# Kernel tuning notes

Hardware: AMD Instinct MI355X
Metric: run time of the kernel (lower is better)

Reference implementation:

```python
import jax, jax.numpy as jnp
import numpy as np
from jax import lax

# Dense emulation of the irregular graph stage (repo helpers img2graph /
# IrregularMaxPool2d / GraphConv2d): nodes = pixels of the stride-4 grid.
# Where pooling_mask==1, a 2x2 block is max-pooled (pooled value replicated
# over the block) and subsequent GraphConv2d gathers neighbors with offset 2
# (dilation 2); where mask==0 the node keeps resolution and offset 1.


def _conv(x, w, b, dil=1):
    p = dil  # SAME padding for a 3x3 kernel with dilation `dil`
    y = lax.conv_general_dilated(x, w, (1, 1), ((p, p), (p, p)),
                                 rhs_dilation=(dil, dil),
                                 dimension_numbers=('NCHW', 'OIHW', 'NCHW'))
    return y + b[None, :, None, None]


def _maxpool2(x):
    return lax.reduce_window(x, -jnp.inf, lax.max, (1, 1, 2, 2), (1, 1, 2, 2), 'VALID')


def _up2(x):
    return jnp.repeat(jnp.repeat(x, 2, axis=2), 2, axis=3)


def setup_inputs() -> dict:
    key = jax.random.key(0)
    ks = jax.random.split(key, 12)
    B, H, W = 4, 384, 384
    inp = {
        'batch': jax.random.normal(ks[0], (B, 3, H, W), jnp.float32),
        'pooling_mask': jax.random.randint(ks[1], (B, 1, H // 8, W // 8), 0, 2, jnp.int32),
    }
    cfg = [(3, 64), (64, 64), (64, 128), (128, 128), (128, 256),
           (256, 256), (256, 256), (256, 512), (512, 512), (512, 512)]
    for i, (cin, cout) in enumerate(cfg):
        scale = float(np.sqrt(2.0 / (cin * 9)))  # He init for 3x3 conv
        inp[f'W{i+1}'] = jax.random.normal(ks[2 + (i % 10)], (cout, cin, 3, 3), jnp.float32) * scale
        inp[f'b{i+1}'] = jnp.zeros((cout,), jnp.float32)
    return inp


def reference(batch, pooling_mask, W1, b1, W2, b2, W3, b3, W4, b4, W5, b5,
              W6, b6, W7, b7, W8, b8, W9, b9, W10, b10):
    x = jax.nn.relu(_conv(batch, W1, b1))
    x = jax.nn.relu(_conv(x, W2, b2))
    x = _maxpool2(x)                                  # H/2
    x = jax.nn.relu(_conv(x, W3, b3))
    x = jax.nn.relu(_conv(x, W4, b4))
    x = _maxpool2(x)                                  # H/4 (OS4)
    x = jax.nn.relu(_conv(x, W5, b5))
    x = jax.nn.relu(_conv(x, W6, b6))
    x = jax.nn.relu(_conv(x, W7, b7))
    # img2graph + IrregularMaxPool2d (number_pools=1)
    m = (pooling_mask > 0).astype(x.dtype)            # [B,1,H/8,W/8]
    m_up = _up2(m)                                    # [B,1,H/4,W/4]
    x = m_up * _up2(_maxpool2(x)) + (1.0 - m_up) * x  # pool 2x2 where mask==1

    # GraphConv2d: per-node neighbor offset = 1 + mask (spatially varying dilation)
    def gconv(h, w, b):
        return m_up * _conv(h, w, b, dil=2) + (1.0 - m_up) * _conv(h, w, b, dil=1)

    x = jax.nn.relu(gconv(x, W8, b8))
    x = jax.nn.relu(gconv(x, W9, b9))
    x = jax.nn.relu(gconv(x, W10, b10))               # use_relu=True
    return x  # graph2img: nodes already laid out on the stride-4 grid
```

## Files before the change

kernel.cpp:

```cpp
#include <hip/hip_runtime.h>


typedef __attribute__((ext_vector_type(8))) short short8;
typedef __attribute__((ext_vector_type(4))) float f32x4;

__device__ __forceinline__ float b2f(ushort u) {
    return __uint_as_float(((unsigned)u) << 16);
}
__device__ __forceinline__ ushort f2b(float f) {
    unsigned x = __float_as_uint(f);
    x += 0x7FFFu + ((x >> 16) & 1u);
    return (ushort)(x >> 16);
}
__device__ __forceinline__ ushort bmax(ushort a, ushort b) {
    return b2f(a) > b2f(b) ? a : b;
}

__global__ __launch_bounds__(256)
void repack_w(const float* __restrict__ w, ushort* __restrict__ wp, int Cin, int Cout)
{
    int n = Cout * Cin * 9;
    int i = blockIdx.x * 256 + threadIdx.x;
    if (i >= n) return;
    int CBl = Cin / 32;
    int c8   = i & 7;
    int co   = (i >> 3) % Cout;
    int rest = (i >> 3) / Cout;
    int q    = rest & 3;
    int cbt  = rest >> 2;
    int cb   = cbt % CBl;
    int t    = cbt / CBl;
    int ci   = cb * 32 + q * 8 + c8;
    wp[i] = f2b(w[((size_t)co * Cin + ci) * 9 + t]);
}

__global__ __launch_bounds__(256)
void l1_conv(const float* __restrict__ in, const float* __restrict__ w,
             const float* __restrict__ bias, ushort* __restrict__ out)
{
    const int H = 384, W = 384;
    __shared__ float s[3][18][18];
    const int tid = threadIdx.x;
    const int tilesX = W / 16;
    const int x0 = (blockIdx.x % tilesX) * 16;
    const int y0 = (blockIdx.x / tilesX) * 16;
    const int b  = blockIdx.z;

    for (int i = tid; i < 3 * 18 * 18; i += 256) {
        int ci = i / (18 * 18);
        int r  = i % (18 * 18);
        int iy = r / 18, ix = r % 18;
        int gy = y0 - 1 + iy, gx = x0 - 1 + ix;
        float v = 0.f;
        if ((unsigned)gy < (unsigned)H && (unsigned)gx < (unsigned)W)
            v = in[((size_t)(b * 3 + ci) * H + gy) * W + gx];
        s[ci][iy][ix] = v;
    }
    __syncthreads();

    const int tx = tid & 15, ty = tid >> 4;
    float iv[3][3][3];
    #pragma unroll
    for (int ci = 0; ci < 3; ++ci)
        #pragma unroll
        for (int ky = 0; ky < 3; ++ky)
            #pragma unroll
            for (int kx = 0; kx < 3; ++kx)
                iv[ci][ky][kx] = s[ci][ty + ky][tx + kx];

    size_t pix = ((size_t)(b * H + y0 + ty) * W + x0 + tx);
    #pragma unroll
    for (int c4 = 0; c4 < 4; ++c4) {
        __align__(16) ushort ob[16];
        #pragma unroll
        for (int co = 0; co < 16; ++co) {
            int coG = c4 * 16 + co;
            float a = bias[coG];
            #pragma unroll
            for (int ci = 0; ci < 3; ++ci)
                #pragma unroll
                for (int ky = 0; ky < 3; ++ky)
                    #pragma unroll
                    for (int kx = 0; kx < 3; ++kx)
                        a = fmaf(w[((size_t)coG * 3 + ci) * 9 + ky * 3 + kx],
                                 iv[ci][ky][kx], a);
            a = a > 0.f ? a : 0.f;
            ob[co] = f2b(a);
        }
        *(short8*)&out[pix * 64 + c4 * 16]     = *(short8*)&ob[0];
        *(short8*)&out[pix * 64 + c4 * 16 + 8] = *(short8*)&ob[8];
    }
}

__global__ __launch_bounds__(256)
void maxpool_nhwc(const ushort* __restrict__ in, ushort* __restrict__ out,
                  int Ho, int Wo, int C)
{
    int n = 4 * Ho * Wo * (C / 8);
    int i = blockIdx.x * 256 + threadIdx.x;
    if (i >= n) return;
    int c8 = i % (C / 8);
    int pi = i / (C / 8);
    int x = pi % Wo, y = (pi / Wo) % Ho, b = pi / (Wo * Ho);
    int Hi = Ho * 2, Wi = Wo * 2;
    const ushort* p = in + ((size_t)(b * Hi + 2 * y) * Wi + 2 * x) * C + c8 * 8;
    short8 v00 = *(const short8*)p;
    short8 v01 = *(const short8*)(p + C);
    short8 v10 = *(const short8*)(p + (size_t)Wi * C);
    short8 v11 = *(const short8*)(p + (size_t)Wi * C + C);
    short8 o;
    #pragma unroll
    for (int j = 0; j < 8; ++j)
        o[j] = (short)bmax(bmax((ushort)v00[j], (ushort)v01[j]),
                           bmax((ushort)v10[j], (ushort)v11[j]));
    *(short8*)(out + (size_t)i * 8) = o;
}

__global__ __launch_bounds__(256)
void irpool_nhwc(const ushort* __restrict__ in, const int* __restrict__ mask,
                 ushort* __restrict__ out)
{
    const int C = 256, H = 96, Wd = 96;
    int n = 4 * H * Wd * (C / 8);
    int i = blockIdx.x * 256 + threadIdx.x;
    if (i >= n) return;
    int c8 = i % (C / 8);
    int pi = i / (C / 8);
    int x = pi % Wd, y = (pi / Wd) % H, b = pi / (Wd * H);
    int m = mask[(b * 48 + (y >> 1)) * 48 + (x >> 1)];
    short8 o;
    if (m) {
        int y0 = y & ~1, x0 = x & ~1;
        const ushort* p = in + ((size_t)(b * H + y0) * Wd + x0) * C + c8 * 8;
        short8 v00 = *(const short8*)p;
        short8 v01 = *(const short8*)(p + C);
        short8 v10 = *(const short8*)(p + (size_t)Wd * C);
        short8 v11 = *(const short8*)(p + (size_t)Wd * C + C);
        #pragma unroll
        for (int j = 0; j < 8; ++j)
            o[j] = (short)bmax(bmax((ushort)v00[j], (ushort)v01[j]),
                               bmax((ushort)v10[j], (ushort)v11[j]));
    } else {
        o = *(const short8*)(in + (size_t)pi * C + c8 * 8);
    }
    *(short8*)(out + (size_t)pi * C + c8 * 8) = o;
}

template<int TR, int BN, int CIN, int COUT, int H, int W, bool GCONV, bool FINAL>
__global__ __launch_bounds__(256)
void conv_mfma(const ushort* __restrict__ in, const ushort* __restrict__ wp,
               const float* __restrict__ bias, void* __restrict__ outv,
               const int* __restrict__ mask)
{
    constexpr int BM   = TR * 16;
    constexpr int CB   = CIN / 32;
    constexpr int HA   = GCONV ? 2 : 1;
    constexpr int CW   = 16 + 2 * HA;
    constexpr int CR   = TR + 2 * HA;
    constexpr int NCH  = CR * CW;
    constexpr int NCHP = NCH + 2;
    constexpr int WM   = BM / 64;
    constexpr int NSA  = NCH * 4;
    constexpr int NSLA = (NSA + 255) / 256;
    constexpr int NSB  = 12 * BN;
    constexpr int NSLB = NSB / 256;
    static_assert(NSB % 256 == 0, "B staging must tile 256 threads");

    __shared__ __align__(16) ushort sA[4 * NCHP * 8];
    __shared__ __align__(16) ushort sB[12 * BN * 8];

    const int tid  = threadIdx.x;
    const int lane = tid & 63;
    const int wv   = tid >> 6;
    const int wm   = wv % WM;
    const int wn   = wv / WM;
    const int col  = lane & 15;
    const int quad = lane >> 4;

    const int tiles_x = W / 16, tiles_y = H / TR;
    int sp = blockIdx.x;
    const int b  = sp / (tiles_x * tiles_y);
    int rr = sp - b * tiles_x * tiles_y;
    const int ty = rr / tiles_x;
    const int tx = rr - ty * tiles_x;
    const int y0 = ty * TR, x0 = tx * 16;
    const int co0 = blockIdx.y * BN;

    int dA[4], aoff[4];
    #pragma unroll
    for (int mt = 0; mt < 4; ++mt) {
        dA[mt] = 1;
        if (GCONV) {
            int y = y0 + wm * 4 + mt, x = x0 + col;
            dA[mt] = mask[(b * (H / 2) + (y >> 1)) * (W / 2) + (x >> 1)] ? 2 : 1;
        }
        aoff[mt] = (HA + wm * 4 + mt) * CW + HA + col;
    }

    short8 pA[NSLA];
    short8 pB[NSLB];

    auto loadA = [&](int cb) {
        #pragma unroll
        for (int k = 0; k < NSLA; ++k) {
            int i = tid + k * 256;
            short8 v = {0, 0, 0, 0, 0, 0, 0, 0};
            if (NSA == NSLA * 256 || i < NSA) {
                int chunk = i >> 2, part = i & 3;
                int yy = chunk / CW, xx = chunk - yy * CW;
                int gy = y0 - HA + yy, gx = x0 - HA + xx;
                if ((unsigned)gy < (unsigned)H && (unsigned)gx < (unsigned)W)
                    v = *(const short8*)(in + ((size_t)(b * H + gy) * W + gx) * CIN
                                         + cb * 32 + part * 8);
            }
            pA[k] = v;
        }
    };
    auto storeA = [&]() {
        #pragma unroll
        for (int k = 0; k < NSLA; ++k) {
            int i = tid + k * 256;
            if (NSA == NSLA * 256 || i < NSA) {
                int chunk = i >> 2, part = i & 3;
                *(short8*)&sA[(part * NCHP + chunk) * 8] = pA[k];
            }
        }
    };
    auto loadB = [&](int s) {
        int cb = s / 3, row = s % 3;
        #pragma unroll
        for (int k = 0; k < NSLB; ++k) {
            int i = tid + k * 256;
            int co = i % BN;
            int rq = i / BN;
            const ushort* gp = wp
                + (((size_t)(row * 3 + (rq >> 2)) * CB + cb) * 4 + (rq & 3))
                      * COUT * 8
                + (size_t)(co0 + co) * 8;
            pB[k] = *(const short8*)gp;
        }
    };
    auto storeB = [&]() {
        #pragma unroll
        for (int k = 0; k < NSLB; ++k) {
            int i = tid + k * 256;
            *(short8*)&sB[(size_t)i * 8] = pB[k];
        }
    };

    f32x4 acc[4][4];
    #pragma unroll
    for (int i = 0; i < 4; ++i)
        #pragma unroll
        for (int j = 0; j < 4; ++j)
            acc[i][j] = (f32x4){0.f, 0.f, 0.f, 0.f};

    loadA(0);
    loadB(0);
    storeA();
    storeB();
    __syncthreads();

    for (int s = 0; s < 3 * CB; ++s) {
        const int row  = s % 3;
        const bool last = (s == 3 * CB - 1);
        if (!last) {
            loadB(s + 1);
            if (row == 2) loadA(s / 3 + 1);
        }
        const int ky = row - 1;
        #pragma unroll
        for (int j = 0; j < 3; ++j) {
            const int kx = j - 1;
            short8 af[4], bf4[4];
            #pragma unroll
            for (int i = 0; i < 4; ++i) {
                int chunk = aoff[i] + dA[i] * (ky * CW + kx);
                af[i]  = *(const short8*)&sA[(quad * NCHP + chunk) * 8];
                bf4[i] = *(const short8*)&sB[((j * 4 + quad) * BN
                                              + wn * 64 + i * 16 + col) * 8];
            }
            #pragma unroll
            for (int mt = 0; mt < 4; ++mt)
                #pragma unroll
                for (int nt = 0; nt < 4; ++nt)
                    acc[mt][nt] = __builtin_amdgcn_mfma_f32_16x16x32_bf16(
                        af[mt], bf4[nt], acc[mt][nt], 0, 0, 0);
        }
        if (!last) {
            __syncthreads();
            storeB();
            if (row == 2) storeA();
            __syncthreads();
        }
    }

    if (!FINAL) {
        ushort* outp = (ushort*)outv;
        #pragma unroll
        for (int mt = 0; mt < 4; ++mt) {
            int y = y0 + wm * 4 + mt;
            #pragma unroll
            for (int nt = 0; nt < 4; ++nt) {
                int co = co0 + wn * 64 + nt * 16 + col;
                float bv = bias[co];
                #pragma unroll
                for (int r2 = 0; r2 < 4; ++r2) {
                    int x = x0 + quad * 4 + r2;
                    float vv = acc[mt][nt][r2] + bv;
                    vv = vv > 0.f ? vv : 0.f;
                    outp[((size_t)(b * H + y) * W + x) * COUT + co] = f2b(vv);
                }
            }
        }
    } else {
        float* outp = (float*)outv;
        #pragma unroll
        for (int mt = 0; mt < 4; ++mt) {
            int y = y0 + wm * 4 + mt;
            #pragma unroll
            for (int nt = 0; nt < 4; ++nt) {
                int co = co0 + wn * 64 + nt * 16 + col;
                float bv = bias[co];
                f32x4 vv;
                #pragma unroll
                for (int r2 = 0; r2 < 4; ++r2) {
                    float z = acc[mt][nt][r2] + bv;
                    vv[r2] = z > 0.f ? z : 0.f;
                }
                *(f32x4*)&outp[((size_t)(b * COUT + co) * H + y) * W + x0 + quad * 4] = vv;
            }
        }
    }
}

extern "C" void kernel_launch(void* const* d_in, const int* in_sizes, int n_in,
                              void* d_out, int out_size, void* d_ws, size_t ws_size,
                              hipStream_t stream)
{
    const float* x    = (const float*)d_in[0];
    const int*   mask = (const int*)d_in[1];
    const float* Wt[10];
    const float* bs[10];
    for (int i = 0; i < 10; ++i) {
        Wt[i] = (const float*)d_in[2 + 2 * i];
        bs[i] = (const float*)d_in[3 + 2 * i];
    }

    const size_t ACT = (size_t)4 * 384 * 384 * 64;
    ushort* A  = (ushort*)d_ws;
    ushort* Bb = A + ACT;
    ushort* wpbase = Bb + ACT;

    static const int cins[10]  = {3, 64, 64, 128, 128, 256, 256, 256, 512, 512};
    static const int couts[10] = {64, 64, 128, 128, 256, 256, 256, 512, 512, 512};
    ushort* wp[10];
    size_t wo = 0;
    for (int l = 1; l < 10; ++l) {
        wp[l] = wpbase + wo;
        wo += (size_t)couts[l] * cins[l] * 9;
    }
    for (int l = 1; l < 10; ++l) {
        int n = couts[l] * cins[l] * 9;
        repack_w<<<(n + 255) / 256, 256, 0, stream>>>(Wt[l], wp[l], cins[l], couts[l]);
    }

    l1_conv<<<dim3(24 * 24, 1, 4), 256, 0, stream>>>(x, Wt[0], bs[0], A);

    conv_mfma<16, 64, 64, 64, 384, 384, false, false>
        <<<dim3(4 * 24 * 24, 1), 256, 0, stream>>>(A, wp[1], bs[1], Bb, nullptr);
    maxpool_nhwc<<<(4 * 192 * 192 * 8 + 255) / 256, 256, 0, stream>>>(Bb, A, 192, 192, 64);

    conv_mfma<8, 128, 64, 128, 192, 192, false, false>
        <<<dim3(4 * 24 * 12, 1), 256, 0, stream>>>(A, wp[2], bs[2], Bb, nullptr);
    conv_mfma<8, 128, 128, 128, 192, 192, false, false>
        <<<dim3(4 * 24 * 12, 1), 256, 0, stream>>>(Bb, wp[3], bs[3], A, nullptr);
    maxpool_nhwc<<<(4 * 96 * 96 * 16 + 255) / 256, 256, 0, stream>>>(A, Bb, 96, 96, 128);

    conv_mfma<8, 128, 128, 256, 96, 96, false, false>
        <<<dim3(4 * 12 * 6, 2), 256, 0, stream>>>(Bb, wp[4], bs[4], A, nullptr);
    conv_mfma<8, 128, 256, 256, 96, 96, false, false>
        <<<dim3(4 * 12 * 6, 2), 256, 0, stream>>>(A, wp[5], bs[5], Bb, nullptr);
    conv_mfma<8, 128, 256, 256, 96, 96, false, false>
        <<<dim3(4 * 12 * 6, 2), 256, 0, stream>>>(Bb, wp[6], bs[6], A, nullptr);

    irpool_nhwc<<<(4 * 96 * 96 * 32 + 255) / 256, 256, 0, stream>>>(A, mask, Bb);

    conv_mfma<8, 128, 256, 512, 96, 96, true, false>
        <<<dim3(4 * 12 * 6, 4), 256, 0, stream>>>(Bb, wp[7], bs[7], A, mask);
    conv_mfma<8, 128, 512, 512, 96, 96, true, false>
        <<<dim3(4 * 12 * 6, 4), 256, 0, stream>>>(A, wp[8], bs[8], Bb, mask);
    conv_mfma<8, 128, 512, 512, 96, 96, true, true>
        <<<dim3(4 * 12 * 6, 4), 256, 0, stream>>>(Bb, wp[9], bs[9], d_out, mask);

    (void)in_sizes; (void)n_in; (void)out_size; (void)ws_size;
}
```

Measured before the change: 957.3 us.

## Load conv weights directly from global into registers, drop shared-memory B staging

Removes the shared-memory staging buffer for weights. Each wave now loads its MFMA B fragments straight from global memory into registers, double-buffered one tap ahead. The loop is restructured to process pairs of input-channel blocks with all 9 taps unrolled, so block-wide barriers only occur at A-tile refills rather than after every kernel row. This cuts LDS traffic and synchronisation, but weights are now fetched redundantly by waves that share output channels (relying on L1/L2), and global-load latency is exposed with only one tap of lookahead.

```diff
diff --git a/kernel.cpp b/kernel.cpp
--- a/kernel.cpp
+++ b/kernel.cpp
@@ -154,6 +154,7 @@
 {
     constexpr int BM   = TR * 16;
     constexpr int CB   = CIN / 32;
+    static_assert(CB % 2 == 0, "cb-pair unroll needs even CB");
     constexpr int HA   = GCONV ? 2 : 1;
     constexpr int CW   = 16 + 2 * HA;
     constexpr int CR   = TR + 2 * HA;
@@ -162,12 +163,8 @@
     constexpr int WM   = BM / 64;
     constexpr int NSA  = NCH * 4;
     constexpr int NSLA = (NSA + 255) / 256;
-    constexpr int NSB  = 12 * BN;
-    constexpr int NSLB = NSB / 256;
-    static_assert(NSB % 256 == 0, "B staging must tile 256 threads");
 
     __shared__ __align__(16) ushort sA[4 * NCHP * 8];
-    __shared__ __align__(16) ushort sB[12 * BN * 8];
 
     const int tid  = threadIdx.x;
     const int lane = tid & 63;
@@ -197,8 +194,9 @@
         aoff[mt] = (HA + wm * 4 + mt) * CW + HA + col;
     }
 
+    const ushort* wbase = wp + ((size_t)quad * COUT + co0 + wn * 64 + col) * 8;
+
     short8 pA[NSLA];
-    short8 pB[NSLB];
 
     auto loadA = [&](int cb) {
         #pragma unroll
@@ -226,26 +224,13 @@
             }
         }
     };
-    auto loadB = [&](int s) {
-        int cb = s / 3, row = s % 3;
-        #pragma unroll
-        for (int k = 0; k < NSLB; ++k) {
-            int i = tid + k * 256;
-            int co = i % BN;
-            int rq = i / BN;
-            const ushort* gp = wp
-                + (((size_t)(row * 3 + (rq >> 2)) * CB + cb) * 4 + (rq & 3))
-                      * COUT * 8
-                + (size_t)(co0 + co) * 8;
-            pB[k] = *(const short8*)gp;
-        }
-    };
-    auto storeB = [&]() {
-        #pragma unroll
-        for (int k = 0; k < NSLB; ++k) {
-            int i = tid + k * 256;
-            *(short8*)&sB[(size_t)i * 8] = pB[k];
-        }
+
+    short8 bfa[4], bfb[4];
+    auto loadBF = [&](int t, int cb, short8 (&dst)[4]) {
+        size_t ofs = (size_t)(t * CB + cb) * 4 * COUT * 8;
+        #pragma unroll
+        for (int nt = 0; nt < 4; ++nt)
+            dst[nt] = *(const short8*)(wbase + ofs + nt * 128);
     };
 
     f32x4 acc[4][4];
@@ -256,41 +241,48 @@
             acc[i][j] = (f32x4){0.f, 0.f, 0.f, 0.f};
 
     loadA(0);
-    loadB(0);
     storeA();
-    storeB();
+    loadBF(0, 0, bfa);
     __syncthreads();
 
-    for (int s = 0; s < 3 * CB; ++s) {
-        const int row  = s % 3;
-        const bool last = (s == 3 * CB - 1);
-        if (!last) {
-            loadB(s + 1);
-            if (row == 2) loadA(s / 3 + 1);
-        }
-        const int ky = row - 1;
-        #pragma unroll
-        for (int j = 0; j < 3; ++j) {
-            const int kx = j - 1;
-            short8 af[4], bf4[4];
+    for (int cb2 = 0; cb2 < CB; cb2 += 2) {
+        loadA(cb2 + 1);
+        #pragma unroll
+        for (int g = 0; g < 18; ++g) {
+            const int tt = (g >= 9) ? g - 9 : g;
+            if (g == 9) {
+                __syncthreads();
+                storeA();
+                __syncthreads();
+                if (cb2 + 2 < CB) loadA(cb2 + 2);
+            }
+            {
+                int gn = g + 1;
+                int cbn = cb2 + (gn >= 9 ? 1 : 0);
+                int tn  = (gn >= 9) ? gn - 9 : gn;
+                if (gn == 18) { cbn = cb2 + 2; tn = 0; }
+                if (cbn < CB) {
+                    if ((g & 1) == 0) loadBF(tn, cbn, bfb);
+                    else              loadBF(tn, cbn, bfa);
+                }
+            }
+            const int ky = tt / 3 - 1, kx = tt % 3 - 1;
+            short8 af[4];
             #pragma unroll
             for (int i = 0; i < 4; ++i) {
                 int chunk = aoff[i] + dA[i] * (ky * CW + kx);
-                af[i]  = *(const short8*)&sA[(quad * NCHP + chunk) * 8];
-                bf4[i] = *(const short8*)&sB[((j * 4 + quad) * BN
-                                              + wn * 64 + i * 16 + col) * 8];
+                af[i] = *(const short8*)&sA[(quad * NCHP + chunk) * 8];
             }
             #pragma unroll
             for (int mt = 0; mt < 4; ++mt)
                 #pragma unroll
                 for (int nt = 0; nt < 4; ++nt)
                     acc[mt][nt] = __builtin_amdgcn_mfma_f32_16x16x32_bf16(
-                        af[mt], bf4[nt], acc[mt][nt], 0, 0, 0);
-        }
-        if (!last) {
+                        af[mt], (g & 1) ? bfb[nt] : bfa[nt], acc[mt][nt], 0, 0, 0);
+        }
+        if (cb2 + 2 < CB) {
             __syncthreads();
-            storeB();
-            if (row == 2) storeA();
+            storeA();
             __syncthreads();
         }
     }
```

Result: slower. 1.114 ms (+16.4%).

## Schedule conv tiles dynamically via per-layer atomic work counters

Applied to the files above, without the earlier changes.

Turns the MFMA conv kernel into a loop in which each block claims output tiles from a global atomic counter instead of deriving its tile from blockIdx. Per-layer counters live in the workspace and are zeroed by a new tiny kernel. The launch grids equal the tile counts, so in practice each block claims about one tile plus a final failing claim. The intent is smoother load balance and dispatch order; the cost is an extra atomic and barrier per tile and a kernel-wide loop that may raise register pressure.

```diff
diff --git a/kernel.cpp b/kernel.cpp
--- a/kernel.cpp
+++ b/kernel.cpp
@@ -15,6 +15,8 @@
 __device__ __forceinline__ ushort bmax(ushort a, ushort b) {
     return b2f(a) > b2f(b) ? a : b;
 }
+
+__global__ void zero_counters(int* __restrict__ c) { c[threadIdx.x] = 0; }
 
 __global__ __launch_bounds__(256)
 void repack_w(const float* __restrict__ w, ushort* __restrict__ wp, int Cin, int Cout)
@@ -150,7 +152,7 @@
 __global__ __launch_bounds__(256)
 void conv_mfma(const ushort* __restrict__ in, const ushort* __restrict__ wp,
                const float* __restrict__ bias, void* __restrict__ outv,
-               const int* __restrict__ mask)
+               const int* __restrict__ mask, int* __restrict__ counter)
 {
     constexpr int BM   = TR * 16;
     constexpr int CB   = CIN / 32;
@@ -165,9 +167,13 @@
     constexpr int NSB  = 12 * BN;
     constexpr int NSLB = NSB / 256;
     static_assert(NSB % 256 == 0, "B staging must tile 256 threads");
+    constexpr int NSP    = 4 * (H / TR) * (W / 16);
+    constexpr int NSLAB  = COUT / BN;
+    constexpr int NTILES = NSP * NSLAB;
 
     __shared__ __align__(16) ushort sA[4 * NCHP * 8];
     __shared__ __align__(16) ushort sB[12 * BN * 8];
+    __shared__ int s_tile;
 
     const int tid  = threadIdx.x;
     const int lane = tid & 63;
@@ -176,159 +182,166 @@
     const int wn   = wv / WM;
     const int col  = lane & 15;
     const int quad = lane >> 4;
-
     const int tiles_x = W / 16, tiles_y = H / TR;
-    int sp = blockIdx.x;
-    const int b  = sp / (tiles_x * tiles_y);
-    int rr = sp - b * tiles_x * tiles_y;
-    const int ty = rr / tiles_x;
-    const int tx = rr - ty * tiles_x;
-    const int y0 = ty * TR, x0 = tx * 16;
-    const int co0 = blockIdx.y * BN;
-
-    int dA[4], aoff[4];
-    #pragma unroll
-    for (int mt = 0; mt < 4; ++mt) {
-        dA[mt] = 1;
-        if (GCONV) {
-            int y = y0 + wm * 4 + mt, x = x0 + col;
-            dA[mt] = mask[(b * (H / 2) + (y >> 1)) * (W / 2) + (x >> 1)] ? 2 : 1;
-        }
-        aoff[mt] = (HA + wm * 4 + mt) * CW + HA + col;
-    }
-
-    short8 pA[NSLA];
-    short8 pB[NSLB];
-
-    auto loadA = [&](int cb) {
-        #pragma unroll
-        for (int k = 0; k < NSLA; ++k) {
-            int i = tid + k * 256;
-            short8 v = {0, 0, 0, 0, 0, 0, 0, 0};
-            if (NSA == NSLA * 256 || i < NSA) {
-                int chunk = i >> 2, part = i & 3;
-                int yy = chunk / CW, xx = chunk - yy * CW;
-                int gy = y0 - HA + yy, gx = x0 - HA + xx;
-                if ((unsigned)gy < (unsigned)H && (unsigned)gx < (unsigned)W)
-                    v = *(const short8*)(in + ((size_t)(b * H + gy) * W + gx) * CIN
-                                         + cb * 32 + part * 8);
-            }
-            pA[k] = v;
-        }
-    };
-    auto storeA = [&]() {
-        #pragma unroll
-        for (int k = 0; k < NSLA; ++k) {
-            int i = tid + k * 256;
-            if (NSA == NSLA * 256 || i < NSA) {
-                int chunk = i >> 2, part = i & 3;
-                *(short8*)&sA[(part * NCHP + chunk) * 8] = pA[k];
-            }
-        }
-    };
-    auto loadB = [&](int s) {
-        int cb = s / 3, row = s % 3;
-        #pragma unroll
-        for (int k = 0; k < NSLB; ++k) {
-            int i = tid + k * 256;
-            int co = i % BN;
-            int rq = i / BN;
-            const ushort* gp = wp
-                + (((size_t)(row * 3 + (rq >> 2)) * CB + cb) * 4 + (rq & 3))
-                      * COUT * 8
-                + (size_t)(co0 + co) * 8;
-            pB[k] = *(const short8*)gp;
-        }
-    };
-    auto storeB = [&]() {
-        #pragma unroll
-        for (int k = 0; k < NSLB; ++k) {
-            int i = tid + k * 256;
-            *(short8*)&sB[(size_t)i * 8] = pB[k];
-        }
-    };
-
-    f32x4 acc[4][4];
-    #pragma unroll
-    for (int i = 0; i < 4; ++i)
-        #pragma unroll
-        for (int j = 0; j < 4; ++j)
-            acc[i][j] = (f32x4){0.f, 0.f, 0.f, 0.f};
-
-    loadA(0);
-    loadB(0);
-    storeA();
-    storeB();
-    __syncthreads();
-
-    for (int s = 0; s < 3 * CB; ++s) {
-        const int row  = s % 3;
-        const bool last = (s == 3 * CB - 1);
-        if (!last) {
-            loadB(s + 1);
-            if (row == 2) loadA(s / 3 + 1);
-        }
-        const int ky = row - 1;
-        #pragma unroll
-        for (int j = 0; j < 3; ++j) {
-            const int kx = j - 1;
-            short8 af[4], bf4[4];
-            #pragma unroll
-            for (int i = 0; i < 4; ++i) {
-                int chunk = aoff[i] + dA[i] * (ky * CW + kx);
-                af[i]  = *(const short8*)&sA[(quad * NCHP + chunk) * 8];
-                bf4[i] = *(const short8*)&sB[((j * 4 + quad) * BN
-                                              + wn * 64 + i * 16 + col) * 8];
-            }
-            #pragma unroll
-            for (int mt = 0; mt < 4; ++mt)
-                #pragma unroll
-                for (int nt = 0; nt < 4; ++nt)
-                    acc[mt][nt] = __builtin_amdgcn_mfma_f32_16x16x32_bf16(
-                        af[mt], bf4[nt], acc[mt][nt], 0, 0, 0);
-        }
-        if (!last) {
-            __syncthreads();
-            storeB();
-            if (row == 2) storeA();
-            __syncthreads();
-        }
-    }
-
-    if (!FINAL) {
-        ushort* outp = (ushort*)outv;
+
+    while (true) {
+        if (tid == 0) s_tile = atomicAdd(counter, 1);
+        __syncthreads();
+        const int t = s_tile;
+        if (t >= NTILES) break;
+
+        const int sp  = t % NSP;
+        const int co0 = (t / NSP) * BN;
+        const int b  = sp / (tiles_x * tiles_y);
+        int rr = sp - b * tiles_x * tiles_y;
+        const int ty = rr / tiles_x;
+        const int tx = rr - ty * tiles_x;
+        const int y0 = ty * TR, x0 = tx * 16;
+
+        int dA[4], aoff[4];
         #pragma unroll
         for (int mt = 0; mt < 4; ++mt) {
-            int y = y0 + wm * 4 + mt;
-            #pragma unroll
-            for (int nt = 0; nt < 4; ++nt) {
-                int co = co0 + wn * 64 + nt * 16 + col;
-                float bv = bias[co];
+            dA[mt] = 1;
+            if (GCONV) {
+                int y = y0 + wm * 4 + mt, x = x0 + col;
+                dA[mt] = mask[(b * (H / 2) + (y >> 1)) * (W / 2) + (x >> 1)] ? 2 : 1;
+            }
+            aoff[mt] = (HA + wm * 4 + mt) * CW + HA + col;
+        }
+
+        short8 pA[NSLA];
+        short8 pB[NSLB];
+
+        auto loadA = [&](int cb) {
+            #pragma unroll
+            for (int k = 0; k < NSLA; ++k) {
+                int i = tid + k * 256;
+                short8 v = {0, 0, 0, 0, 0, 0, 0, 0};
+                if (NSA == NSLA * 256 || i < NSA) {
+                    int chunk = i >> 2, part = i & 3;
+                    int yy = chunk / CW, xx = chunk - yy * CW;
+                    int gy = y0 - HA + yy, gx = x0 - HA + xx;
+                    if ((unsigned)gy < (unsigned)H && (unsigned)gx < (unsigned)W)
+                        v = *(const short8*)(in + ((size_t)(b * H + gy) * W + gx) * CIN
+                                             + cb * 32 + part * 8);
+                }
+                pA[k] = v;
+            }
+        };
+        auto storeA = [&]() {
+            #pragma unroll
+            for (int k = 0; k < NSLA; ++k) {
+                int i = tid + k * 256;
+                if (NSA == NSLA * 256 || i < NSA) {
+                    int chunk = i >> 2, part = i & 3;
+                    *(short8*)&sA[(part * NCHP + chunk) * 8] = pA[k];
+                }
+            }
+        };
+        auto loadB = [&](int s) {
+            int cb = s / 3, row = s % 3;
+            #pragma unroll
+            for (int k = 0; k < NSLB; ++k) {
+                int i = tid + k * 256;
+                int co = i % BN;
+                int rq = i / BN;
+                const ushort* gp = wp
+                    + (((size_t)(row * 3 + (rq >> 2)) * CB + cb) * 4 + (rq & 3))
+                          * COUT * 8
+                    + (size_t)(co0 + co) * 8;
+                pB[k] = *(const short8*)gp;
+            }
+        };
+        auto storeB = [&]() {
+            #pragma unroll
+            for (int k = 0; k < NSLB; ++k) {
+                int i = tid + k * 256;
+                *(short8*)&sB[(size_t)i * 8] = pB[k];
+            }
+        };
+
+        f32x4 acc[4][4];
+        #pragma unroll
+        for (int i = 0; i < 4; ++i)
+            #pragma unroll
+            for (int j = 0; j < 4; ++j)
+                acc[i][j] = (f32x4){0.f, 0.f, 0.f, 0.f};
+
+        loadA(0);
+        loadB(0);
+        storeA();
+        storeB();
+        __syncthreads();
+
+        for (int s = 0; s < 3 * CB; ++s) {
+            const int row  = s % 3;
+            const bool last = (s == 3 * CB - 1);
+            if (!last) {
+                loadB(s + 1);
+                if (row == 2) loadA(s / 3 + 1);
+            }
+            const int ky = row - 1;
+            #pragma unroll
+            for (int j = 0; j < 3; ++j) {
+                const int kx = j - 1;
+                short8 af[4], bf4[4];
                 #pragma unroll
-                for (int r2 = 0; r2 < 4; ++r2) {
-                    int x = x0 + quad * 4 + r2;
-                    float vv = acc[mt][nt][r2] + bv;
-                    vv = vv > 0.f ? vv : 0.f;
-                    outp[((size_t)(b * H + y) * W + x) * COUT + co] = f2b(vv);
+                for (int i = 0; i < 4; ++i) {
+                    int chunk = aoff[i] + dA[i] * (ky * CW + kx);
+                    af[i]  = *(const short8*)&sA[(quad * NCHP + chunk) * 8];
+                    bf4[i] = *(const short8*)&sB[((j * 4 + quad) * BN
+                                                  + wn * 64 + i * 16 + col) * 8];
                 }
+                #pragma unroll
+                for (int mt = 0; mt < 4; ++mt)
+                    #pragma unroll
+                    for (int nt = 0; nt < 4; ++nt)
+                        acc[mt][nt] = __builtin_amdgcn_mfma_f32_16x16x32_bf16(
+                            af[mt], bf4[nt], acc[mt][nt], 0, 0, 0);
+            }
+            if (!last) {
+                __syncthreads();
+                storeB();
+                if (row == 2) storeA();
+                __syncthreads();
             }
         }
-    } else {
-        float* outp = (float*)outv;
-        #pragma unroll
-        for (int mt = 0; mt < 4; ++mt) {
-            int y = y0 + wm * 4 + mt;
-            #pragma unroll
-            for (int nt = 0; nt < 4; ++nt) {
-                int co = co0 + wn * 64 + nt * 16 + col;
-                float bv = bias[co];
-                f32x4 vv;
+
+        if (!FINAL) {
+            ushort* outp = (ushort*)outv;
+            #pragma unroll
+            for (int mt = 0; mt < 4; ++mt) {
+                int y = y0 + wm * 4 + mt;
                 #pragma unroll
-                for (int r2 = 0; r2 < 4; ++r2) {
-                    float z = acc[mt][nt][r2] + bv;
-                    vv[r2] = z > 0.f ? z : 0.f;
+                for (int nt = 0; nt < 4; ++nt) {
+                    int co = co0 + wn * 64 + nt * 16 + col;
+                    float bv = bias[co];
+                    #pragma unroll
+                    for (int r2 = 0; r2 < 4; ++r2) {
+                        int x = x0 + quad * 4 + r2;
+                        float vv = acc[mt][nt][r2] + bv;
+                        vv = vv > 0.f ? vv : 0.f;
+                        outp[((size_t)(b * H + y) * W + x) * COUT + co] = f2b(vv);
+                    }
                 }
-                *(f32x4*)&outp[((size_t)(b * COUT + co) * H + y) * W + x0 + quad * 4] = vv;
+            }
+        } else {
+            float* outp = (float*)outv;
+            #pragma unroll
+            for (int mt = 0; mt < 4; ++mt) {
+                int y = y0 + wm * 4 + mt;
+                #pragma unroll
+                for (int nt = 0; nt < 4; ++nt) {
+                    int co = co0 + wn * 64 + nt * 16 + col;
+                    float bv = bias[co];
+                    f32x4 vv;
+                    #pragma unroll
+                    for (int r2 = 0; r2 < 4; ++r2) {
+                        float z = acc[mt][nt][r2] + bv;
+                        vv[r2] = z > 0.f ? z : 0.f;
+                    }
+                    *(f32x4*)&outp[((size_t)(b * COUT + co) * H + y) * W + x0 + quad * 4] = vv;
+                }
             }
         }
     }
@@ -360,38 +373,41 @@
         wp[l] = wpbase + wo;
         wo += (size_t)couts[l] * cins[l] * 9;
     }
+    int* counters = (int*)(wpbase + ((wo + 1) & ~(size_t)1));
+
     for (int l = 1; l < 10; ++l) {
         int n = couts[l] * cins[l] * 9;
         repack_w<<<(n + 255) / 256, 256, 0, stream>>>(Wt[l], wp[l], cins[l], couts[l]);
     }
+    zero_counters<<<1, 16, 0, stream>>>(counters);
 
     l1_conv<<<dim3(24 * 24, 1, 4), 256, 0, stream>>>(x, Wt[0], bs[0], A);
 
     conv_mfma<16, 64, 64, 64, 384, 384, false, false>
-        <<<dim3(4 * 24 * 24, 1), 256, 0, stream>>>(A, wp[1], bs[1], Bb, nullptr);
+        <<<dim3(2304), 256, 0, stream>>>(A, wp[1], bs[1], Bb, nullptr, counters + 0);
     maxpool_nhwc<<<(4 * 192 * 192 * 8 + 255) / 256, 256, 0, stream>>>(Bb, A, 192, 192, 64);
 
     conv_mfma<8, 128, 64, 128, 192, 192, false, false>
-        <<<dim3(4 * 24 * 12, 1), 256, 0, stream>>>(A, wp[2], bs[2], Bb, nullptr);
+        <<<dim3(1152), 256, 0, stream>>>(A, wp[2], bs[2], Bb, nullptr, counters + 1);
     conv_mfma<8, 128, 128, 128, 192, 192, false, false>
-        <<<dim3(4 * 24 * 12, 1), 256, 0, stream>>>(Bb, wp[3], bs[3], A, nullptr);
+        <<<dim3(1152), 256, 0, stream>>>(Bb, wp[3], bs[3], A, nullptr, counters + 2);
     maxpool_nhwc<<<(4 * 96 * 96 * 16 + 255) / 256, 256, 0, stream>>>(A, Bb, 96, 96, 128);
 
     conv_mfma<8, 128, 128, 256, 96, 96, false, false>
-        <<<dim3(4 * 12 * 6, 2), 256, 0, stream>>>(Bb, wp[4], bs[4], A, nullptr);
+        <<<dim3(576), 256, 0, stream>>>(Bb, wp[4], bs[4], A, nullptr, counters + 3);
     conv_mfma<8, 128, 256, 256, 96, 96, false, false>
-        <<<dim3(4 * 12 * 6, 2), 256, 0, stream>>>(A, wp[5], bs[5], Bb, nullptr);
+        <<<dim3(576), 256, 0, stream>>>(A, wp[5], bs[5], Bb, nullptr, counters + 4);
     conv_mfma<8, 128, 256, 256, 96, 96, false, false>
-        <<<dim3(4 * 12 * 6, 2), 256, 0, stream>>>(Bb, wp[6], bs[6], A, nullptr);
+        <<<dim3(576), 256, 0, stream>>>(Bb, wp[6], bs[6], A, nullptr, counters + 5);
 
     irpool_nhwc<<<(4 * 96 * 96 * 32 + 255) / 256, 256, 0, stream>>>(A, mask, Bb);
 
     conv_mfma<8, 128, 256, 512, 96, 96, true, false>
-        <<<dim3(4 * 12 * 6, 4), 256, 0, stream>>>(Bb, wp[7], bs[7], A, mask);
+        <<<dim3(1152), 256, 0, stream>>>(Bb, wp[7], bs[7], A, mask, counters + 6);
     conv_mfma<8, 128, 512, 512, 96, 96, true, false>
-        <<<dim3(4 * 12 * 6, 4), 256, 0, stream>>>(A, wp[8], bs[8], Bb, mask);
+        <<<dim3(1152), 256, 0, stream>>>(A, wp[8], bs[8], Bb, mask, counters + 7);
     conv_mfma<8, 128, 512, 512, 96, 96, true, true>
-        <<<dim3(4 * 12 * 6, 4), 256, 0, stream>>>(Bb, wp[9], bs[9], d_out, mask);
+        <<<dim3(1152), 256, 0, stream>>>(Bb, wp[9], bs[9], d_out, mask, counters + 8);
 
     (void)in_sizes; (void)n_in; (void)out_size; (void)ws_size;
 }
```

New measurement: 1.017 ms. 1.06x slower.

## Fuse maxpool and irregular pool into conv epilogues; batch weight repacks

Applied to the files above, without the earlier changes.

Removes the separate maxpool and irregular-pool kernels by doing the 2x2 max inside the conv epilogue. Each wave's accumulator tile already covers aligned 2x2 pixel blocks, and the mask is read per block for the irregular pool. It also merges the nine per-layer weight repack launches into one kernel that takes a struct of per-layer pointers and offsets. This saves full activation round-trips through memory and several kernel launches, at the cost of scattered 2-byte stores in the pooled epilogue.

```diff
diff --git a/kernel.cpp b/kernel.cpp
--- a/kernel.cpp
+++ b/kernel.cpp
@@ -15,23 +15,36 @@
 __device__ __forceinline__ ushort bmax(ushort a, ushort b) {
     return b2f(a) > b2f(b) ? a : b;
 }
+__device__ __forceinline__ float fmaxf2(float a, float b) { return a > b ? a : b; }
+
+struct RepackArgs {
+    const float* w[9];
+    ushort*      wp[9];
+    int cin[9];
+    int cout[9];
+    int off[10];
+};
 
 __global__ __launch_bounds__(256)
-void repack_w(const float* __restrict__ w, ushort* __restrict__ wp, int Cin, int Cout)
+void repack_all(RepackArgs a)
 {
-    int n = Cout * Cin * 9;
     int i = blockIdx.x * 256 + threadIdx.x;
-    if (i >= n) return;
-    int CBl = Cin / 32;
-    int c8   = i & 7;
-    int co   = (i >> 3) % Cout;
-    int rest = (i >> 3) / Cout;
+    if (i >= a.off[9]) return;
+    int l = 0;
+    #pragma unroll
+    for (int k = 1; k < 9; ++k) l += (i >= a.off[k]);
+    int j = i - a.off[l];
+    int Cin = a.cin[l], Cout = a.cout[l];
+    int CBl  = Cin / 32;
+    int c8   = j & 7;
+    int co   = (j >> 3) % Cout;
+    int rest = (j >> 3) / Cout;
     int q    = rest & 3;
     int cbt  = rest >> 2;
     int cb   = cbt % CBl;
     int t    = cbt / CBl;
     int ci   = cb * 32 + q * 8 + c8;
-    wp[i] = f2b(w[((size_t)co * Cin + ci) * 9 + t]);
+    a.wp[l][j] = f2b(a.w[l][((size_t)co * Cin + ci) * 9 + t]);
 }
 
 __global__ __launch_bounds__(256)
@@ -92,61 +105,8 @@
     }
 }
 
-__global__ __launch_bounds__(256)
-void maxpool_nhwc(const ushort* __restrict__ in, ushort* __restrict__ out,
-                  int Ho, int Wo, int C)
-{
-    int n = 4 * Ho * Wo * (C / 8);
-    int i = blockIdx.x * 256 + threadIdx.x;
-    if (i >= n) return;
-    int c8 = i % (C / 8);
-    int pi = i / (C / 8);
-    int x = pi % Wo, y = (pi / Wo) % Ho, b = pi / (Wo * Ho);
-    int Hi = Ho * 2, Wi = Wo * 2;
-    const ushort* p = in + ((size_t)(b * Hi + 2 * y) * Wi + 2 * x) * C + c8 * 8;
-    short8 v00 = *(const short8*)p;
-    short8 v01 = *(const short8*)(p + C);
-    short8 v10 = *(const short8*)(p + (size_t)Wi * C);
-    short8 v11 = *(const short8*)(p + (size_t)Wi * C + C);
-    short8 o;
-    #pragma unroll
-    for (int j = 0; j < 8; ++j)
-        o[j] = (short)bmax(bmax((ushort)v00[j], (ushort)v01[j]),
-                           bmax((ushort)v10[j], (ushort)v11[j]));
-    *(short8*)(out + (size_t)i * 8) = o;
-}
-
-__global__ __launch_bounds__(256)
-void irpool_nhwc(const ushort* __restrict__ in, const int* __restrict__ mask,
-                 ushort* __restrict__ out)
-{
-    const int C = 256, H = 96, Wd = 96;
-    int n = 4 * H * Wd * (C / 8);
-    int i = blockIdx.x * 256 + threadIdx.x;
-    if (i >= n) return;
-    int c8 = i % (C / 8);
-    int pi = i / (C / 8);
-    int x = pi % Wd, y = (pi / Wd) % H, b = pi / (Wd * H);
-    int m = mask[(b * 48 + (y >> 1)) * 48 + (x >> 1)];
-    short8 o;
-    if (m) {
-        int y0 = y & ~1, x0 = x & ~1;
-        const ushort* p = in + ((size_t)(b * H + y0) * Wd + x0) * C + c8 * 8;
-        short8 v00 = *(const short8*)p;
-        short8 v01 = *(const short8*)(p + C);
-        short8 v10 = *(const short8*)(p + (size_t)Wd * C);
-        short8 v11 = *(const short8*)(p + (size_t)Wd * C + C);
-        #pragma unroll
-        for (int j = 0; j < 8; ++j)
-            o[j] = (short)bmax(bmax((ushort)v00[j], (ushort)v01[j]),
-                               bmax((ushort)v10[j], (ushort)v11[j]));
-    } else {
-        o = *(const short8*)(in + (size_t)pi * C + c8 * 8);
-    }
-    *(short8*)(out + (size_t)pi * C + c8 * 8) = o;
-}
-
-template<int TR, int BN, int CIN, int COUT, int H, int W, bool GCONV, bool FINAL>
+template<int TR, int BN, int CIN, int COUT, int H, int W, bool GCONV, bool FINAL,
+         int POOL>
 __global__ __launch_bounds__(256)
 void conv_mfma(const ushort* __restrict__ in, const ushort* __restrict__ wp,
                const float* __restrict__ bias, void* __restrict__ outv,
@@ -295,7 +255,25 @@
         }
     }
 
-    if (!FINAL) {
+    if (FINAL) {
+        float* outp = (float*)outv;
+        #pragma unroll
+        for (int mt = 0; mt < 4; ++mt) {
+            int y = y0 + wm * 4 + mt;
+            #pragma unroll
+            for (int nt = 0; nt < 4; ++nt) {
+                int co = co0 + wn * 64 + nt * 16 + col;
+                float bv = bias[co];
+                f32x4 vv;
+                #pragma unroll
+                for (int r2 = 0; r2 < 4; ++r2) {
+                    float z = acc[mt][nt][r2] + bv;
+                    vv[r2] = z > 0.f ? z : 0.f;
+                }
+                *(f32x4*)&outp[((size_t)(b * COUT + co) * H + y) * W + x0 + quad * 4] = vv;
+            }
+        }
+    } else if (POOL == 0) {
         ushort* outp = (ushort*)outv;
         #pragma unroll
         for (int mt = 0; mt < 4; ++mt) {
@@ -313,22 +291,66 @@
                 }
             }
         }
-    } else {
-        float* outp = (float*)outv;
-        #pragma unroll
-        for (int mt = 0; mt < 4; ++mt) {
-            int y = y0 + wm * 4 + mt;
-            #pragma unroll
-            for (int nt = 0; nt < 4; ++nt) {
-                int co = co0 + wn * 64 + nt * 16 + col;
-                float bv = bias[co];
-                f32x4 vv;
+    } else if (POOL == 1) {
+        ushort* outp = (ushort*)outv;
+        #pragma unroll
+        for (int nt = 0; nt < 4; ++nt) {
+            int co = co0 + wn * 64 + nt * 16 + col;
+            float bv = bias[co];
+            float v[4][4];
+            #pragma unroll
+            for (int mt = 0; mt < 4; ++mt)
                 #pragma unroll
                 for (int r2 = 0; r2 < 4; ++r2) {
                     float z = acc[mt][nt][r2] + bv;
-                    vv[r2] = z > 0.f ? z : 0.f;
-                }
-                *(f32x4*)&outp[((size_t)(b * COUT + co) * H + y) * W + x0 + quad * 4] = vv;
+                    v[mt][r2] = z > 0.f ? z : 0.f;
+                }
+            #pragma unroll
+            for (int mt2 = 0; mt2 < 2; ++mt2) {
+                int yp = (y0 >> 1) + wm * 2 + mt2;
+                #pragma unroll
+                for (int j = 0; j < 2; ++j) {
+                    int xp = (x0 >> 1) + quad * 2 + j;
+                    float m = fmaxf2(fmaxf2(v[2*mt2][2*j],   v[2*mt2][2*j+1]),
+                                     fmaxf2(v[2*mt2+1][2*j], v[2*mt2+1][2*j+1]));
+                    outp[((size_t)(b * (H/2) + yp) * (W/2) + xp) * COUT + co] = f2b(m);
+                }
+            }
+        }
+    } else {
+        ushort* outp = (ushort*)outv;
+        int mc[2][2];
+        #pragma unroll
+        for (int my = 0; my < 2; ++my)
+            #pragma unroll
+            for (int mx = 0; mx < 2; ++mx) {
+                int y = y0 + wm * 4 + my * 2;
+                int x = x0 + quad * 4 + mx * 2;
+                mc[my][mx] = mask[(b * (H / 2) + (y >> 1)) * (W / 2) + (x >> 1)];
+            }
+        #pragma unroll
+        for (int nt = 0; nt < 4; ++nt) {
+            int co = co0 + wn * 64 + nt * 16 + col;
+            float bv = bias[co];
+            float v[4][4];
+            #pragma unroll
+            for (int mt = 0; mt < 4; ++mt)
+                #pragma unroll
+                for (int r2 = 0; r2 < 4; ++r2) {
+                    float z = acc[mt][nt][r2] + bv;
+                    v[mt][r2] = z > 0.f ? z : 0.f;
+                }
+            #pragma unroll
+            for (int mt = 0; mt < 4; ++mt) {
+                int y = y0 + wm * 4 + mt;
+                #pragma unroll
+                for (int r2 = 0; r2 < 4; ++r2) {
+                    int x = x0 + quad * 4 + r2;
+                    float p = fmaxf2(fmaxf2(v[mt][r2],     v[mt][r2 ^ 1]),
+                                     fmaxf2(v[mt ^ 1][r2], v[mt ^ 1][r2 ^ 1]));
+                    float o = mc[mt >> 1][r2 >> 1] ? p : v[mt][r2];
+                    outp[((size_t)(b * H + y) * W + x) * COUT + co] = f2b(o);
+                }
             }
         }
     }
@@ -360,38 +382,43 @@
         wp[l] = wpbase + wo;
         wo += (size_t)couts[l] * cins[l] * 9;
     }
+
+    RepackArgs ra;
+    int off = 0;
     for (int l = 1; l < 10; ++l) {
-        int n = couts[l] * cins[l] * 9;
-        repack_w<<<(n + 255) / 256, 256, 0, stream>>>(Wt[l], wp[l], cins[l], couts[l]);
-    }
+        ra.w[l - 1]    = Wt[l];
+        ra.wp[l - 1]   = wp[l];
+        ra.cin[l - 1]  = cins[l];
+        ra.cout[l - 1] = couts[l];
+        ra.off[l - 1]  = off;
+        off += couts[l] * cins[l] * 9;
+    }
+    ra.off[9] = off;
+    repack_all<<<(off + 255) / 256, 256, 0, stream>>>(ra);
 
     l1_conv<<<dim3(24 * 24, 1, 4), 256, 0, stream>>>(x, Wt[0], bs[0], A);
 
-    conv_mfma<16, 64, 64, 64, 384, 384, false, false>
+    conv_mfma<16, 64, 64, 64, 384, 384, false, false, 1>
         <<<dim3(4 * 24 * 24, 1), 256, 0, stream>>>(A, wp[1], bs[1], Bb, nullptr);
-    maxpool_nhwc<<<(4 * 192 * 192 * 8 + 255) / 256, 256, 0, stream>>>(Bb, A, 192, 192, 64);
-
-    conv_mfma<8, 128, 64, 128, 192, 192, false, false>
-        <<<dim3(4 * 24 * 12, 1), 256, 0, stream>>>(A, wp[2], bs[2], Bb, nullptr);
-    conv_mfma<8, 128, 128, 128, 192, 192, false, false>
-        <<<dim3(4 * 24 * 12, 1), 256, 0, stream>>>(Bb, wp[3], bs[3], A, nullptr);
-    maxpool_nhwc<<<(4 * 96 * 96 * 16 + 255) / 256, 256, 0, stream>>>(A, Bb, 96, 96, 128);
-
-    conv_mfma<8, 128, 128, 256, 96, 96, false, false>
+
+    conv_mfma<8, 128, 64, 128, 192, 192, false, false, 0>
+        <<<dim3(4 * 24 * 12, 1), 256, 0, stream>>>(Bb, wp[2], bs[2], A, nullptr);
+    conv_mfma<8, 128, 128, 128, 192, 192, false, false, 1>
+        <<<dim3(4 * 24 * 12, 1), 256, 0, stream>>>(A, wp[3], bs[3], Bb, nullptr);
+
+    conv_mfma<8, 128, 128, 256, 96, 96, false, false, 0>
         <<<dim3(4 * 12 * 6, 2), 256, 0, stream>>>(Bb, wp[4], bs[4], A, nullptr);
-    conv_mfma<8, 128, 256, 256, 96, 96, false, false>
+    conv_mfma<8, 128, 256, 256, 96, 96, false, false, 0>
         <<<dim3(4 * 12 * 6, 2), 256, 0, stream>>>(A, wp[5], bs[5], Bb, nullptr);
-    conv_mfma<8, 128, 256, 256, 96, 96, false, false>
-        <<<dim3(4 * 12 * 6, 2), 256, 0, stream>>>(Bb, wp[6], bs[6], A, nullptr);
-
-    irpool_nhwc<<<(4 * 96 * 96 * 32 + 255) / 256, 256, 0, stream>>>(A, mask, Bb);
-
-    conv_mfma<8, 128, 256, 512, 96, 96, true, false>
-        <<<dim3(4 * 12 * 6, 4), 256, 0, stream>>>(Bb, wp[7], bs[7], A, mask);
-    conv_mfma<8, 128, 512, 512, 96, 96, true, false>
-        <<<dim3(4 * 12 * 6, 4), 256, 0, stream>>>(A, wp[8], bs[8], Bb, mask);
-    conv_mfma<8, 128, 512, 512, 96, 96, true, true>
-        <<<dim3(4 * 12 * 6, 4), 256, 0, stream>>>(Bb, wp[9], bs[9], d_out, mask);
+    conv_mfma<8, 128, 256, 256, 96, 96, false, false, 2>
+        <<<dim3(4 * 12 * 6, 2), 256, 0, stream>>>(Bb, wp[6], bs[6], A, mask);
+
+    conv_mfma<8, 128, 256, 512, 96, 96, true, false, 0>
+        <<<dim3(4 * 12 * 6, 4), 256, 0, stream>>>(A, wp[7], bs[7], Bb, mask);
+    conv_mfma<8, 128, 512, 512, 96, 96, true, false, 0>
+        <<<dim3(4 * 12 * 6, 4), 256, 0, stream>>>(Bb, wp[8], bs[8], A, mask);
+    conv_mfma<8, 128, 512, 512, 96, 96, true, true, 0>
+        <<<dim3(4 * 12 * 6, 4), 256, 0, stream>>>(A, wp[9], bs[9], d_out, mask);
 
     (void)in_sizes; (void)n_in; (void)out_size; (void)ws_size;
 }
```

After: 899.7 us. 1.06x faster.
